# Kernel optimization log

Hardware: AMD Instinct MI355X
Metric: run time of the kernel (lower is better)

The kernel has to match this reference:

```python
import jax, jax.numpy as jnp
import numpy as np

C = 512
GROUPS = 32
EPS = 1e-6

def setup_inputs() -> dict:
    key = jax.random.key(0)
    ks = jax.random.split(key, 6)
    s = 1.0 / np.sqrt(C)
    return {
        "x": jax.random.normal(ks[0], (2, C, 16, 32, 32), dtype=jnp.float32),
        "gamma": jnp.ones((C,), jnp.float32),
        "beta": jnp.zeros((C,), jnp.float32),
        "q_w": jax.random.normal(ks[1], (C, C), jnp.float32) * s,
        "q_b": jnp.zeros((C,), jnp.float32),
        "k_w": jax.random.normal(ks[2], (C, C), jnp.float32) * s,
        "k_b": jnp.zeros((C,), jnp.float32),
        "v_w": jax.random.normal(ks[3], (C, C), jnp.float32) * s,
        "v_b": jnp.zeros((C,), jnp.float32),
        "proj_w": jax.random.normal(ks[4], (C, C), jnp.float32) * s,
        "proj_b": jnp.zeros((C,), jnp.float32),
    }

def _group_norm(x, gamma, beta):
    # x: [b, c, t, h, w]
    b, c, t, h, w = x.shape
    xg = x.reshape(b, GROUPS, c // GROUPS, t, h, w)
    mean = xg.mean(axis=(2, 3, 4, 5), keepdims=True)
    var = xg.var(axis=(2, 3, 4, 5), keepdims=True)
    xg = (xg - mean) * jax.lax.rsqrt(var + EPS)
    x = xg.reshape(b, c, t, h, w)
    return x * gamma[None, :, None, None, None] + beta[None, :, None, None, None]

def _pw_conv(x, w, bias):
    # 1x1x1 conv == channel GEMM. x: [b,c,t,h,w], w: [c_out, c_in]
    y = jnp.einsum('bcthw,oc->bothw', x, w)
    return y + bias[None, :, None, None, None]

def reference(x, gamma, beta, q_w, q_b, k_w, k_b, v_w, v_b, proj_w, proj_b):
    b, c, t, h, w = x.shape
    hn = _group_norm(x, gamma, beta)
    q = _pw_conv(hn, q_w, q_b)
    k = _pw_conv(hn, k_w, k_b)
    v = _pw_conv(hn, v_w, v_b)
    # [b,c,t,h,w] -> [b*t, h*w, c]
    def to_seq(a):
        return jnp.transpose(a, (0, 2, 3, 4, 1)).reshape(b * t, h * w, c)
    q, k, v = to_seq(q), to_seq(k), to_seq(v)
    scale = 1.0 / jnp.sqrt(jnp.asarray(c, x.dtype))
    attn = jnp.einsum('bqc,bkc->bqk', q, k) * scale  # [b*t, hw, hw]
    attn = jax.nn.softmax(attn, axis=-1)
    out = jnp.einsum('bqk,bkc->bqc', attn, v)
    out = out.reshape(b, t, h, w, c).transpose(0, 4, 1, 2, 3)
    return x + _pw_conv(out, proj_w, proj_b)
```

## Files before the change

kernel.cpp:

```cpp
#include <hip/hip_runtime.h>

typedef unsigned short u16;
typedef __attribute__((ext_vector_type(8))) short bf16x8;
typedef __attribute__((ext_vector_type(4))) float f32x4;

#define DEV static __device__ __forceinline__

DEV u16 f2bf(float f) {
  union { float f; unsigned u; } x; x.f = f;
  return (u16)((x.u + 0x7FFFu + ((x.u >> 16) & 1u)) >> 16);
}
DEV float bf2f(u16 h) { union { unsigned u; float f; } x; x.u = ((unsigned)h) << 16; return x.f; }

DEV void gload16(const void* g, void* l) {
  __builtin_amdgcn_global_load_lds((const __attribute__((address_space(1))) void*)g,
                                   (__attribute__((address_space(3))) void*)l, 16, 0, 0);
}

DEV int eswz(int r) { return (((r & 7) ^ ((r >> 3) & 7)) << 4); }

__global__ __launch_bounds__(256) void gn_stats_a(const float* __restrict__ x,
                                                  float2* __restrict__ part) {
  const int bg = blockIdx.x >> 5, slice = blockIdx.x & 31;
  const float* base = x + (long)bg * 262144 + slice * 8192;
  float s = 0.f, q = 0.f;
#pragma unroll
  for (int i = 0; i < 8; ++i) {
    float4 v = *(const float4*)(base + i * 1024 + threadIdx.x * 4);
    s += v.x + v.y + v.z + v.w;
    q += v.x * v.x + v.y * v.y + v.z * v.z + v.w * v.w;
  }
#pragma unroll
  for (int o = 32; o; o >>= 1) { s += __shfl_xor(s, o); q += __shfl_xor(q, o); }
  __shared__ float2 red[4];
  if ((threadIdx.x & 63) == 0) red[threadIdx.x >> 6] = make_float2(s, q);
  __syncthreads();
  if (threadIdx.x == 0) {
    float S = 0.f, Q = 0.f;
    for (int i = 0; i < 4; ++i) { S += red[i].x; Q += red[i].y; }
    part[blockIdx.x] = make_float2(S, Q);
  }
}

__global__ void gn_stats_b(const float2* __restrict__ part, float2* __restrict__ stats) {
  float s = 0.f, q = 0.f;
  if (threadIdx.x < 32) {
    float2 p = part[blockIdx.x * 32 + threadIdx.x];
    s = p.x; q = p.y;
  }
#pragma unroll
  for (int o = 32; o; o >>= 1) { s += __shfl_xor(s, o); q += __shfl_xor(q, o); }
  if (threadIdx.x == 0) {
    const float inv = 1.f / 262144.f;
    float mean = s * inv;
    float var = q * inv - mean * mean;
    stats[blockIdx.x] = make_float2(mean, rsqrtf(var + 1e-6f));
  }
}

__global__ __launch_bounds__(256) void gn_apply(const float* __restrict__ x,
                                                const float* __restrict__ gamma,
                                                const float* __restrict__ beta,
                                                const float2* __restrict__ stats,
                                                u16* __restrict__ hn) {
  __shared__ u16 tile[64][65];
  const int p0 = blockIdx.x * 64, c0 = blockIdx.y * 64, bt = blockIdx.z;
  const int b = bt >> 4, t = bt & 15, tid = threadIdx.x;
  const float* xb = x + (long)b * 8388608 + t * 1024;
#pragma unroll 4
  for (int r = 0; r < 16; ++r) {
    int ci = r * 4 + (tid >> 6), pi = tid & 63;
    int c = c0 + ci;
    float2 st = stats[b * 32 + (c >> 4)];
    float v = xb[(long)c * 16384 + p0 + pi];
    v = (v - st.x) * st.y * gamma[c] + beta[c];
    tile[ci][pi] = f2bf(v);
  }
  __syncthreads();
  u16* hb = hn + ((long)bt * 1024 + p0) * 512 + c0;
#pragma unroll 4
  for (int r = 0; r < 16; ++r) {
    int pi = r * 4 + (tid >> 6), ci = tid & 63;
    hb[(long)pi * 512 + ci] = tile[ci][pi];
  }
}

__global__ __launch_bounds__(256) void wconv(const float* __restrict__ w0, const float* __restrict__ w1,
                                             const float* __restrict__ w2, const float* __restrict__ w3,
                                             u16* __restrict__ dst) {
  int e = (blockIdx.x * 256 + threadIdx.x) * 4;
  const float* src = w0;
  int which = e >> 18, off = e & 262143;
  if (which == 1) src = w1; else if (which == 2) src = w2; else if (which == 3) src = w3;
  float4 v = *(const float4*)(src + off);
  ushort4 o;
  o.x = f2bf(v.x); o.y = f2bf(v.y); o.z = f2bf(v.z); o.w = f2bf(v.w);
  *(ushort4*)(dst + e) = o;
}

__global__ void bcat(const float* __restrict__ qb, const float* __restrict__ kb,
                     const float* __restrict__ vb, float* __restrict__ dst) {
  int i = blockIdx.x * 256 + threadIdx.x;
  if (i < 512) dst[i] = qb[i];
  else if (i < 1024) dst[i] = kb[i - 512];
  else if (i < 1536) dst[i] = vb[i - 1024];
}

__global__ __launch_bounds__(256) void softmax_rows_bf16(u16* __restrict__ scores) {
  const int wave = threadIdx.x >> 6, lane = threadIdx.x & 63;
  const long row = (long)blockIdx.x * 4 + wave;
  u16* srow = scores + row * 1024;
  bf16x8 a0 = *(const bf16x8*)(srow + lane * 16);
  bf16x8 a1 = *(const bf16x8*)(srow + lane * 16 + 8);
  float v[16];
#pragma unroll
  for (int j = 0; j < 8; ++j) { v[j] = bf2f((u16)a0[j]); v[8 + j] = bf2f((u16)a1[j]); }
  float m = v[0];
#pragma unroll
  for (int j = 1; j < 16; ++j) m = fmaxf(m, v[j]);
#pragma unroll
  for (int o = 32; o; o >>= 1) m = fmaxf(m, __shfl_xor(m, o));
  const float sc = 0.044194173824159216f;
  float s = 0.f, e[16];
#pragma unroll
  for (int j = 0; j < 16; ++j) { e[j] = __expf((v[j] - m) * sc); s += e[j]; }
#pragma unroll
  for (int o = 32; o; o >>= 1) s += __shfl_xor(s, o);
  const float inv = 1.f / s;
  bf16x8 o0, o1;
#pragma unroll
  for (int j = 0; j < 8; ++j) {
    o0[j] = (short)f2bf(e[j] * inv);
    o1[j] = (short)f2bf(e[8 + j] * inv);
  }
  *(bf16x8*)(srow + lane * 16) = o0;
  *(bf16x8*)(srow + lane * 16 + 8) = o1;
}

template <int EPI>
__global__ __launch_bounds__(512, 4) void gemmk(
    const u16* __restrict__ A, int lda, long sA,
    const u16* __restrict__ B, int ldb, long sB,
    u16* __restrict__ Cv, int ldc, long sC,
    const float* __restrict__ bias, int K,
    const float* __restrict__ xin, float* __restrict__ outp,
    u16* __restrict__ vT) {
  __shared__ u16 sm[3 * 12288];
  char* smc = (char*)sm;
  const int tid = threadIdx.x, wid = tid >> 6, lane = tid & 63;
  const int wm = wid >> 2, wn = wid & 3;

  int bx = blockIdx.x, by = blockIdx.y, bz = blockIdx.z;
  {
    unsigned gx = gridDim.x, gy = gridDim.y;
    unsigned total = gx * gy * gridDim.z;
    if ((total & 7u) == 0) {
      unsigned gxy = gx * gy;
      unsigned d = (blockIdx.z * gy + blockIdx.y) * gx + blockIdx.x;
      unsigned w = (d & 7u) * (total >> 3) + (d >> 3);
      bz = w / gxy; unsigned r = w - (unsigned)bz * gxy;
      bx = r / gy;  by = r - (unsigned)bx * gy;
    }
  }
  const long m0 = (long)bx * 128, n0 = (long)by * 256;
  const char* Ab = (const char*)(A + (long)bz * sA + m0 * lda);
  const char* Bb = (const char*)(B + (long)bz * sB + n0 * ldb);
  const int NT = K >> 5;
  const long lda2 = 2L * lda, ldb2 = 2L * ldb;

  const int srow = tid >> 2;
  const int cb = ((tid & 3) * 16) ^ ((srow & 3) << 4);
  const int dA = srow * 64 + (tid & 3) * 16;
  const int dB0 = 8192 + dA, dB1 = 16384 + dA;
  const char* gA  = Ab + (long)srow * lda2 + cb;
  const char* gB0 = Bb + (long)srow * ldb2 + cb;
  const char* gB1 = Bb + (long)(srow + 128) * ldb2 + cb;

  const int lrow = lane & 15, kslot = (lane >> 4) * 16;
  const int aoff = (wm * 64 + lrow) * 64 + (kslot ^ ((lrow & 3) << 4));
  const int boff = 8192 + (wn * 64 + lrow) * 64 + (kslot ^ ((lrow & 3) << 4));

  f32x4 acc[4][4] = {};

#define STG3(off) do { gload16(gA, smc + (off) + dA); \
                       gload16(gB0, smc + (off) + dB0); \
                       gload16(gB1, smc + (off) + dB1); } while (0)

  STG3(0);
  gA += 64; gB0 += 64; gB1 += 64;
  if (NT > 1) { STG3(24576); gA += 64; gB0 += 64; gB1 += 64; }
  if (NT > 1) asm volatile("s_waitcnt vmcnt(3)" ::: "memory");
  else        asm volatile("s_waitcnt vmcnt(0)" ::: "memory");
  __builtin_amdgcn_s_barrier();

  int cb_cur = 0, cb_stg = 49152;
  for (int T = 0; T < NT; ++T) {
    const bool s2 = (T + 2 < NT);
    if (s2) { STG3(cb_stg); gA += 64; gB0 += 64; gB1 += 64; }
    const char* ba = smc + cb_cur;
    bf16x8 af[4], bf[4];
#pragma unroll
    for (int mi = 0; mi < 4; ++mi) af[mi] = *(const bf16x8*)(ba + aoff + mi * 1024);
#pragma unroll
    for (int ni = 0; ni < 4; ++ni) bf[ni] = *(const bf16x8*)(ba + boff + ni * 1024);
    __builtin_amdgcn_s_setprio(1);
#pragma unroll
    for (int mi = 0; mi < 4; ++mi)
#pragma unroll
      for (int ni = 0; ni < 4; ++ni)
        acc[mi][ni] = __builtin_amdgcn_mfma_f32_16x16x32_bf16(af[mi], bf[ni], acc[mi][ni], 0, 0, 0);
    __builtin_amdgcn_s_setprio(0);
    if (s2) asm volatile("s_waitcnt vmcnt(3)" ::: "memory");
    else    asm volatile("s_waitcnt vmcnt(0)" ::: "memory");
    __builtin_amdgcn_s_barrier();
    cb_cur = (cb_cur == 49152) ? 0 : cb_cur + 24576;
    cb_stg = (cb_stg == 49152) ? 0 : cb_stg + 24576;
  }
#undef STG3

  __syncthreads();
  {
    const int lc = lane & 15, lr = (lane >> 4) * 4;
    char* wb_ = smc + wid * 8192;
#pragma unroll
    for (int ni = 0; ni < 4; ++ni) {
      float bv = 0.f;
      if (EPI == 1) bv = bias[n0 + wn * 64 + ni * 16 + lc];
#pragma unroll
      for (int mi = 0; mi < 4; ++mi)
#pragma unroll
        for (int j = 0; j < 4; ++j) {
          int rml = mi * 16 + lr + j;
          int colb = (ni * 32 + lc * 2) ^ eswz(rml);
          *(u16*)(wb_ + rml * 128 + colb) = f2bf(acc[mi][ni][j] + bv);
        }
    }
  }
  __syncthreads();

  if (EPI == 2) {
    const int bt = (int)(m0 >> 10), p0i = (int)(m0 & 1023);
    const int b = bt >> 4, t = bt & 15;
    const int p8 = (tid & 15) * 8, cl = tid >> 4;
#pragma unroll
    for (int ci = 0; ci < 8; ++ci) {
      int c = ci * 32 + cl;
      const long base = (long)b * 8388608 + (long)(n0 + c) * 16384 + t * 1024 + p0i + p8;
      const float bv = bias[n0 + c];
      const int reg = (((p8 >> 6) << 2) | (c >> 6)) * 8192;
      const int c2 = (c & 63) * 2;
      float vals[8];
#pragma unroll
      for (int j = 0; j < 8; ++j) {
        int r = (p8 + j) & 63;
        vals[j] = bf2f(*(const u16*)(smc + reg + r * 128 + (c2 ^ eswz(r))));
      }
      float4 x0 = *(const float4*)(xin + base);
      float4 x1 = *(const float4*)(xin + base + 4);
      float4 o0 = make_float4(x0.x + bv + vals[0], x0.y + bv + vals[1],
                              x0.z + bv + vals[2], x0.w + bv + vals[3]);
      float4 o1 = make_float4(x1.x + bv + vals[4], x1.y + bv + vals[5],
                              x1.z + bv + vals[6], x1.w + bv + vals[7]);
      *(float4*)(outp + base) = o0;
      *(float4*)(outp + base + 4) = o1;
    }
  } else if (EPI == 1 && n0 >= 1024) {
    const int bt = (int)(m0 >> 10), p0i = (int)(m0 & 1023);
    const int p8 = (tid & 15) * 8, cl = tid >> 4;
    u16* vbase = vT + (long)bt * 524288 + (long)(n0 - 1024) * 1024 + p0i;
#pragma unroll
    for (int ci = 0; ci < 8; ++ci) {
      int c = ci * 32 + cl;
      const int reg = (((p8 >> 6) << 2) | (c >> 6)) * 8192;
      const int c2 = (c & 63) * 2;
      u16 tmp[8];
#pragma unroll
      for (int j = 0; j < 8; ++j) {
        int r = (p8 + j) & 63;
        tmp[j] = *(const u16*)(smc + reg + r * 128 + (c2 ^ eswz(r)));
      }
      *(bf16x8*)(vbase + (long)c * 1024 + p8) = *(bf16x8*)tmp;
    }
  } else {
    u16* C = Cv + (long)bz * sC;
    const int c8 = tid & 31, r0e = tid >> 5;
#pragma unroll
    for (int i = 0; i < 8; ++i) {
      int r = r0e + i * 16;
      int rwid = ((r >> 6) << 2) | (c8 >> 3);
      int rr = r & 63;
      bf16x8 v = *(const bf16x8*)(smc + rwid * 8192 + rr * 128 +
                                  (((c8 & 7) * 16) ^ eswz(rr)));
      *(bf16x8*)(C + (m0 + r) * (long)ldc + n0 + c8 * 8) = v;
    }
  }
}

extern "C" void kernel_launch(void* const* d_in, const int* in_sizes, int n_in,
                              void* d_out, int out_size, void* d_ws, size_t ws_size,
                              hipStream_t stream) {
  (void)in_sizes; (void)n_in; (void)out_size;
  const float* x      = (const float*)d_in[0];
  const float* gamma  = (const float*)d_in[1];
  const float* beta   = (const float*)d_in[2];
  const float* q_w    = (const float*)d_in[3];
  const float* q_b    = (const float*)d_in[4];
  const float* k_w    = (const float*)d_in[5];
  const float* k_b    = (const float*)d_in[6];
  const float* v_w    = (const float*)d_in[7];
  const float* v_b    = (const float*)d_in[8];
  const float* proj_w = (const float*)d_in[9];
  const float* proj_b = (const float*)d_in[10];

  const size_t OFF_WB    = 0;
  const size_t OFF_BIAS  = 2097152;
  const size_t OFF_STATS = 2103296;
  const size_t OFF_PART  = 2103808;
  const size_t OFF_HN    = 2121728;
  const size_t OFF_QK    = 35676160;
  const size_t OFF_VT    = 102785024;
  const size_t OFF_SC    = 136339456;

  char* ws = (char*)d_ws;
  u16*    wb      = (u16*)(ws + OFF_WB);
  float*  qkvbias = (float*)(ws + OFF_BIAS);
  float2* stats   = (float2*)(ws + OFF_STATS);
  float2* part    = (float2*)(ws + OFF_PART);
  u16*    hn      = (u16*)(ws + OFF_HN);
  u16*    ob      = hn;
  u16*    qk      = (u16*)(ws + OFF_QK);
  u16*    vT      = (u16*)(ws + OFF_VT);
  u16*    scores  = (u16*)(ws + OFF_SC);

  const int CH = (ws_size >= OFF_SC + 32ULL * 2097152) ? 32 : 8;

  wconv<<<1024, 256, 0, stream>>>(q_w, k_w, v_w, proj_w, wb);
  bcat<<<6, 256, 0, stream>>>(q_b, k_b, v_b, qkvbias);
  gn_stats_a<<<2048, 256, 0, stream>>>(x, part);
  gn_stats_b<<<64, 64, 0, stream>>>(part, stats);
  gn_apply<<<dim3(16, 8, 32), 256, 0, stream>>>(x, gamma, beta, stats, hn);

  gemmk<1><<<dim3(256, 6, 1), 512, 0, stream>>>(
      hn, 512, 0, wb, 512, 0, qk, 1024, 0, qkvbias, 512, nullptr, nullptr, vT);

  for (int ch = 0; ch < 32 / CH; ++ch) {
    long f0 = (long)ch * CH;
    gemmk<0><<<dim3(8, 4, CH), 512, 0, stream>>>(
        qk + f0 * 1048576, 1024, 1048576,
        qk + 512 + f0 * 1048576, 1024, 1048576,
        scores, 1024, 1048576, nullptr, 512, nullptr, nullptr, nullptr);
    softmax_rows_bf16<<<CH * 256, 256, 0, stream>>>(scores);
    gemmk<0><<<dim3(8, 2, CH), 512, 0, stream>>>(
        scores, 1024, 1048576,
        vT + f0 * 524288, 1024, 524288,
        ob + f0 * 524288, 512, 524288, nullptr, 1024, nullptr, nullptr, nullptr);
  }

  gemmk<2><<<dim3(256, 2, 1), 512, 0, stream>>>(
      ob, 512, 0, wb + 786432, 512, 0, nullptr, 0, 0, proj_b, 512,
      x, (float*)d_out, nullptr);
}
```

Baseline: 269.0 us.

## Fuse softmax normalization into PV GEMM A-load using precomputed row stats

Replaces the in-place softmax pass with a stats-only kernel that writes per-row max and inverse sum. The PV GEMM then loads raw scores through registers and applies exp/normalize before writing them to shared memory. This drops the separate read-modify-write of the full score matrix, at the cost of extra exp work and register-path loads inside the GEMM pipeline. It also merges the weight and bias prep kernels into one launch, and removes both the block-index swizzle and the setprio hints from the GEMM, which could change cache locality and scheduling.

```diff
diff --git a/kernel.cpp b/kernel.cpp
--- a/kernel.cpp
+++ b/kernel.cpp
@@ -18,6 +18,8 @@
 }
 
 DEV int eswz(int r) { return (((r & 7) ^ ((r >> 3) & 7)) << 4); }
+
+#define SM_SCALE 0.044194173824159216f
 
 __global__ __launch_bounds__(256) void gn_stats_a(const float* __restrict__ x,
                                                   float2* __restrict__ part) {
@@ -85,25 +87,26 @@
   }
 }
 
-__global__ __launch_bounds__(256) void wconv(const float* __restrict__ w0, const float* __restrict__ w1,
-                                             const float* __restrict__ w2, const float* __restrict__ w3,
-                                             u16* __restrict__ dst) {
-  int e = (blockIdx.x * 256 + threadIdx.x) * 4;
-  const float* src = w0;
-  int which = e >> 18, off = e & 262143;
-  if (which == 1) src = w1; else if (which == 2) src = w2; else if (which == 3) src = w3;
-  float4 v = *(const float4*)(src + off);
-  ushort4 o;
-  o.x = f2bf(v.x); o.y = f2bf(v.y); o.z = f2bf(v.z); o.w = f2bf(v.w);
-  *(ushort4*)(dst + e) = o;
-}
-
-__global__ void bcat(const float* __restrict__ qb, const float* __restrict__ kb,
-                     const float* __restrict__ vb, float* __restrict__ dst) {
-  int i = blockIdx.x * 256 + threadIdx.x;
-  if (i < 512) dst[i] = qb[i];
-  else if (i < 1024) dst[i] = kb[i - 512];
-  else if (i < 1536) dst[i] = vb[i - 1024];
+__global__ __launch_bounds__(256) void prep(const float* __restrict__ w0, const float* __restrict__ w1,
+                                            const float* __restrict__ w2, const float* __restrict__ w3,
+                                            const float* __restrict__ qb, const float* __restrict__ kb,
+                                            const float* __restrict__ vb,
+                                            u16* __restrict__ dst, float* __restrict__ bias) {
+  if (blockIdx.x < 1024) {
+    int e = (blockIdx.x * 256 + threadIdx.x) * 4;
+    const float* src = w0;
+    int which = e >> 18, off = e & 262143;
+    if (which == 1) src = w1; else if (which == 2) src = w2; else if (which == 3) src = w3;
+    float4 v = *(const float4*)(src + off);
+    ushort4 o;
+    o.x = f2bf(v.x); o.y = f2bf(v.y); o.z = f2bf(v.z); o.w = f2bf(v.w);
+    *(ushort4*)(dst + e) = o;
+  } else {
+    for (int i = threadIdx.x; i < 1536; i += 256) {
+      float v = (i < 512) ? qb[i] : (i < 1024) ? kb[i - 512] : vb[i - 1024];
+      bias[i] = v;
+    }
+  }
 }
 
 __global__ __launch_bounds__(256) void softmax_rows_bf16(u16* __restrict__ scores) {
@@ -120,10 +123,9 @@
   for (int j = 1; j < 16; ++j) m = fmaxf(m, v[j]);
 #pragma unroll
   for (int o = 32; o; o >>= 1) m = fmaxf(m, __shfl_xor(m, o));
-  const float sc = 0.044194173824159216f;
   float s = 0.f, e[16];
 #pragma unroll
-  for (int j = 0; j < 16; ++j) { e[j] = __expf((v[j] - m) * sc); s += e[j]; }
+  for (int j = 0; j < 16; ++j) { e[j] = __expf((v[j] - m) * SM_SCALE); s += e[j]; }
 #pragma unroll
   for (int o = 32; o; o >>= 1) s += __shfl_xor(s, o);
   const float inv = 1.f / s;
@@ -137,31 +139,46 @@
   *(bf16x8*)(srow + lane * 16 + 8) = o1;
 }
 
-template <int EPI>
+__global__ __launch_bounds__(256) void sm_stats(const u16* __restrict__ scores,
+                                                float2* __restrict__ rowstats) {
+  const int wave = threadIdx.x >> 6, lane = threadIdx.x & 63;
+  const long row = (long)blockIdx.x * 4 + wave;
+  const u16* srow = scores + row * 1024;
+  bf16x8 a0 = *(const bf16x8*)(srow + lane * 16);
+  bf16x8 a1 = *(const bf16x8*)(srow + lane * 16 + 8);
+  float v[16];
+#pragma unroll
+  for (int j = 0; j < 8; ++j) {
+    v[j] = bf2f((u16)a0[j]) * SM_SCALE;
+    v[8 + j] = bf2f((u16)a1[j]) * SM_SCALE;
+  }
+  float m = v[0];
+#pragma unroll
+  for (int j = 1; j < 16; ++j) m = fmaxf(m, v[j]);
+#pragma unroll
+  for (int o = 32; o; o >>= 1) m = fmaxf(m, __shfl_xor(m, o));
+  float s = 0.f;
+#pragma unroll
+  for (int j = 0; j < 16; ++j) s += __expf(v[j] - m);
+#pragma unroll
+  for (int o = 32; o; o >>= 1) s += __shfl_xor(s, o);
+  if (lane == 0) rowstats[row] = make_float2(m, 1.f / s);
+}
+
+template <int EPI, int ASRC>
 __global__ __launch_bounds__(512, 4) void gemmk(
     const u16* __restrict__ A, int lda, long sA,
     const u16* __restrict__ B, int ldb, long sB,
     u16* __restrict__ Cv, int ldc, long sC,
     const float* __restrict__ bias, int K,
     const float* __restrict__ xin, float* __restrict__ outp,
-    u16* __restrict__ vT) {
+    u16* __restrict__ vT, const float2* __restrict__ rowstats) {
   __shared__ u16 sm[3 * 12288];
   char* smc = (char*)sm;
   const int tid = threadIdx.x, wid = tid >> 6, lane = tid & 63;
   const int wm = wid >> 2, wn = wid & 3;
 
-  int bx = blockIdx.x, by = blockIdx.y, bz = blockIdx.z;
-  {
-    unsigned gx = gridDim.x, gy = gridDim.y;
-    unsigned total = gx * gy * gridDim.z;
-    if ((total & 7u) == 0) {
-      unsigned gxy = gx * gy;
-      unsigned d = (blockIdx.z * gy + blockIdx.y) * gx + blockIdx.x;
-      unsigned w = (d & 7u) * (total >> 3) + (d >> 3);
-      bz = w / gxy; unsigned r = w - (unsigned)bz * gxy;
-      bx = r / gy;  by = r - (unsigned)bx * gy;
-    }
-  }
+  const int bx = blockIdx.x, by = blockIdx.y, bz = blockIdx.z;
   const long m0 = (long)bx * 128, n0 = (long)by * 256;
   const char* Ab = (const char*)(A + (long)bz * sA + m0 * lda);
   const char* Bb = (const char*)(B + (long)bz * sB + n0 * ldb);
@@ -171,8 +188,8 @@
   const int srow = tid >> 2;
   const int cb = ((tid & 3) * 16) ^ ((srow & 3) << 4);
   const int dA = srow * 64 + (tid & 3) * 16;
+  const int dAsw = srow * 64 + cb;
   const int dB0 = 8192 + dA, dB1 = 16384 + dA;
-  const char* gA  = Ab + (long)srow * lda2 + cb;
   const char* gB0 = Bb + (long)srow * ldb2 + cb;
   const char* gB1 = Bb + (long)(srow + 128) * ldb2 + cb;
 
@@ -182,41 +199,94 @@
 
   f32x4 acc[4][4] = {};
 
+  if (ASRC == 0) {
+    const char* gA = Ab + (long)srow * lda2 + cb;
 #define STG3(off) do { gload16(gA, smc + (off) + dA); \
                        gload16(gB0, smc + (off) + dB0); \
                        gload16(gB1, smc + (off) + dB1); } while (0)
-
-  STG3(0);
-  gA += 64; gB0 += 64; gB1 += 64;
-  if (NT > 1) { STG3(24576); gA += 64; gB0 += 64; gB1 += 64; }
-  if (NT > 1) asm volatile("s_waitcnt vmcnt(3)" ::: "memory");
-  else        asm volatile("s_waitcnt vmcnt(0)" ::: "memory");
-  __builtin_amdgcn_s_barrier();
-
-  int cb_cur = 0, cb_stg = 49152;
-  for (int T = 0; T < NT; ++T) {
-    const bool s2 = (T + 2 < NT);
-    if (s2) { STG3(cb_stg); gA += 64; gB0 += 64; gB1 += 64; }
-    const char* ba = smc + cb_cur;
-    bf16x8 af[4], bf[4];
-#pragma unroll
-    for (int mi = 0; mi < 4; ++mi) af[mi] = *(const bf16x8*)(ba + aoff + mi * 1024);
-#pragma unroll
-    for (int ni = 0; ni < 4; ++ni) bf[ni] = *(const bf16x8*)(ba + boff + ni * 1024);
-    __builtin_amdgcn_s_setprio(1);
-#pragma unroll
-    for (int mi = 0; mi < 4; ++mi)
-#pragma unroll
-      for (int ni = 0; ni < 4; ++ni)
-        acc[mi][ni] = __builtin_amdgcn_mfma_f32_16x16x32_bf16(af[mi], bf[ni], acc[mi][ni], 0, 0, 0);
-    __builtin_amdgcn_s_setprio(0);
-    if (s2) asm volatile("s_waitcnt vmcnt(3)" ::: "memory");
-    else    asm volatile("s_waitcnt vmcnt(0)" ::: "memory");
+    STG3(0);
+    gA += 64; gB0 += 64; gB1 += 64;
+    if (NT > 1) { STG3(24576); gA += 64; gB0 += 64; gB1 += 64; }
+    if (NT > 1) asm volatile("s_waitcnt vmcnt(3)" ::: "memory");
+    else        asm volatile("s_waitcnt vmcnt(0)" ::: "memory");
     __builtin_amdgcn_s_barrier();
-    cb_cur = (cb_cur == 49152) ? 0 : cb_cur + 24576;
-    cb_stg = (cb_stg == 49152) ? 0 : cb_stg + 24576;
-  }
+
+    int cb_cur = 0, cb_stg = 49152;
+    for (int T = 0; T < NT; ++T) {
+      const bool s2 = (T + 2 < NT);
+      if (s2) { STG3(cb_stg); gA += 64; gB0 += 64; gB1 += 64; }
+      const char* ba = smc + cb_cur;
+      bf16x8 af[4], bf[4];
+#pragma unroll
+      for (int mi = 0; mi < 4; ++mi) af[mi] = *(const bf16x8*)(ba + aoff + mi * 1024);
+#pragma unroll
+      for (int ni = 0; ni < 4; ++ni) bf[ni] = *(const bf16x8*)(ba + boff + ni * 1024);
+#pragma unroll
+      for (int mi = 0; mi < 4; ++mi)
+#pragma unroll
+        for (int ni = 0; ni < 4; ++ni)
+          acc[mi][ni] = __builtin_amdgcn_mfma_f32_16x16x32_bf16(af[mi], bf[ni], acc[mi][ni], 0, 0, 0);
+      if (s2) asm volatile("s_waitcnt vmcnt(3)" ::: "memory");
+      else    asm volatile("s_waitcnt vmcnt(0)" ::: "memory");
+      __builtin_amdgcn_s_barrier();
+      cb_cur = (cb_cur == 49152) ? 0 : cb_cur + 24576;
+      cb_stg = (cb_stg == 49152) ? 0 : cb_stg + 24576;
+    }
 #undef STG3
+  } else {
+    const float2 rs = rowstats[(long)bz * 1024 + m0 + srow];
+    const float mneg = -rs.x, invS = rs.y;
+    const u16* gAr = A + (long)bz * sA + (m0 + srow) * (long)lda + (tid & 3) * 8;
+    bf16x8 aCur;
+#define STGB(off) do { gload16(gB0, smc + (off) + dB0); \
+                       gload16(gB1, smc + (off) + dB1); } while (0)
+#define XFORM(dstoff) do { u16 tmp_[8]; \
+      _Pragma("unroll") \
+      for (int j_ = 0; j_ < 8; ++j_) { \
+        float f_ = bf2f((u16)aCur[j_]); \
+        tmp_[j_] = f2bf(__expf(fmaf(f_, SM_SCALE, mneg)) * invS); \
+      } \
+      *(bf16x8*)(smc + (dstoff) + dAsw) = *(bf16x8*)tmp_; } while (0)
+
+    aCur = *(const bf16x8*)gAr;
+    STGB(0);
+    gB0 += 64; gB1 += 64;
+    if (NT > 1) { STGB(24576); gB0 += 64; gB1 += 64; }
+    if (NT > 1) asm volatile("s_waitcnt vmcnt(2)" ::: "memory");
+    else        asm volatile("s_waitcnt vmcnt(0)" ::: "memory");
+    XFORM(0);
+    asm volatile("s_waitcnt lgkmcnt(0)" ::: "memory");
+    __builtin_amdgcn_s_barrier();
+
+    int cb_cur = 0, cb_nxt = 24576, cb_stg = 49152;
+    for (int T = 0; T < NT; ++T) {
+      const bool s1 = (T + 1 < NT), s2 = (T + 2 < NT);
+      bf16x8 aNext;
+      if (s1) aNext = *(const bf16x8*)(gAr + (T + 1) * 32);
+      if (s2) { STGB(cb_stg); gB0 += 64; gB1 += 64; }
+      const char* ba = smc + cb_cur;
+      bf16x8 af[4], bf[4];
+#pragma unroll
+      for (int mi = 0; mi < 4; ++mi) af[mi] = *(const bf16x8*)(ba + aoff + mi * 1024);
+#pragma unroll
+      for (int ni = 0; ni < 4; ++ni) bf[ni] = *(const bf16x8*)(ba + boff + ni * 1024);
+#pragma unroll
+      for (int mi = 0; mi < 4; ++mi)
+#pragma unroll
+        for (int ni = 0; ni < 4; ++ni)
+          acc[mi][ni] = __builtin_amdgcn_mfma_f32_16x16x32_bf16(af[mi], bf[ni], acc[mi][ni], 0, 0, 0);
+      if (s2)      asm volatile("s_waitcnt vmcnt(2)" ::: "memory");
+      else         asm volatile("s_waitcnt vmcnt(0)" ::: "memory");
+      if (s1) { aCur = aNext; XFORM(cb_nxt); }
+      asm volatile("s_waitcnt lgkmcnt(0)" ::: "memory");
+      __builtin_amdgcn_s_barrier();
+      cb_cur = cb_nxt;
+      cb_nxt = cb_stg;
+      cb_stg = (cb_stg == 49152) ? 0 : cb_stg + 24576;
+    }
+#undef STGB
+#undef XFORM
+  }
 
   __syncthreads();
   {
@@ -320,6 +390,7 @@
   const size_t OFF_QK    = 35676160;
   const size_t OFF_VT    = 102785024;
   const size_t OFF_SC    = 136339456;
+  const size_t OFF_RS    = 203448320;
 
   char* ws = (char*)d_ws;
   u16*    wb      = (u16*)(ws + OFF_WB);
@@ -331,32 +402,41 @@
   u16*    qk      = (u16*)(ws + OFF_QK);
   u16*    vT      = (u16*)(ws + OFF_VT);
   u16*    scores  = (u16*)(ws + OFF_SC);
-
-  const int CH = (ws_size >= OFF_SC + 32ULL * 2097152) ? 32 : 8;
-
-  wconv<<<1024, 256, 0, stream>>>(q_w, k_w, v_w, proj_w, wb);
-  bcat<<<6, 256, 0, stream>>>(q_b, k_b, v_b, qkvbias);
+  float2* rowstats = (float2*)(ws + OFF_RS);
+
+  const bool FUSED = (ws_size >= OFF_RS + 262144);
+  const int CH = FUSED ? 32 : 8;
+
+  prep<<<1025, 256, 0, stream>>>(q_w, k_w, v_w, proj_w, q_b, k_b, v_b, wb, qkvbias);
   gn_stats_a<<<2048, 256, 0, stream>>>(x, part);
   gn_stats_b<<<64, 64, 0, stream>>>(part, stats);
   gn_apply<<<dim3(16, 8, 32), 256, 0, stream>>>(x, gamma, beta, stats, hn);
 
-  gemmk<1><<<dim3(256, 6, 1), 512, 0, stream>>>(
-      hn, 512, 0, wb, 512, 0, qk, 1024, 0, qkvbias, 512, nullptr, nullptr, vT);
+  gemmk<1, 0><<<dim3(256, 6, 1), 512, 0, stream>>>(
+      hn, 512, 0, wb, 512, 0, qk, 1024, 0, qkvbias, 512, nullptr, nullptr, vT, nullptr);
 
   for (int ch = 0; ch < 32 / CH; ++ch) {
     long f0 = (long)ch * CH;
-    gemmk<0><<<dim3(8, 4, CH), 512, 0, stream>>>(
+    gemmk<0, 0><<<dim3(8, 4, CH), 512, 0, stream>>>(
         qk + f0 * 1048576, 1024, 1048576,
         qk + 512 + f0 * 1048576, 1024, 1048576,
-        scores, 1024, 1048576, nullptr, 512, nullptr, nullptr, nullptr);
-    softmax_rows_bf16<<<CH * 256, 256, 0, stream>>>(scores);
-    gemmk<0><<<dim3(8, 2, CH), 512, 0, stream>>>(
-        scores, 1024, 1048576,
-        vT + f0 * 524288, 1024, 524288,
-        ob + f0 * 524288, 512, 524288, nullptr, 1024, nullptr, nullptr, nullptr);
-  }
-
-  gemmk<2><<<dim3(256, 2, 1), 512, 0, stream>>>(
+        scores, 1024, 1048576, nullptr, 512, nullptr, nullptr, nullptr, nullptr);
+    if (FUSED) {
+      sm_stats<<<CH * 256, 256, 0, stream>>>(scores, rowstats);
+      gemmk<0, 1><<<dim3(8, 2, CH), 512, 0, stream>>>(
+          scores, 1024, 1048576,
+          vT + f0 * 524288, 1024, 524288,
+          ob + f0 * 524288, 512, 524288, nullptr, 1024, nullptr, nullptr, nullptr, rowstats);
+    } else {
+      softmax_rows_bf16<<<CH * 256, 256, 0, stream>>>(scores);
+      gemmk<0, 0><<<dim3(8, 2, CH), 512, 0, stream>>>(
+          scores, 1024, 1048576,
+          vT + f0 * 524288, 1024, 524288,
+          ob + f0 * 524288, 512, 524288, nullptr, 1024, nullptr, nullptr, nullptr, nullptr);
+    }
+  }
+
+  gemmk<2, 0><<<dim3(256, 2, 1), 512, 0, stream>>>(
       ob, 512, 0, wb + 786432, 512, 0, nullptr, 0, 0, proj_b, 512,
-      x, (float*)d_out, nullptr);
-}
+      x, (float*)d_out, nullptr, nullptr);
+}
```

After: 285.5 us. +6.1%, slower.
